# Performance work log

Hardware: AMD Instinct MI355X
Metric: run time of the kernel (lower is better)

The kernel has to match this reference:

```python
import jax, jax.numpy as jnp
import numpy as np

D_MODEL = 1024
N_HEADS = 16
D_K = D_MODEL // N_HEADS


def setup_inputs() -> dict:
    key = jax.random.key(0)
    ks = jax.random.split(key, 12)
    B, S = 4, 2048
    sc = 1.0 / np.sqrt(D_MODEL)
    inp = {
        "query": jax.random.normal(ks[0], (B, S, D_MODEL), jnp.float32),
        "key": jax.random.normal(ks[1], (B, S, D_MODEL), jnp.float32),
        "value": jax.random.normal(ks[2], (B, S, D_MODEL), jnp.float32),
        "Wq": jax.random.normal(ks[3], (D_MODEL, D_MODEL), jnp.float32) * sc,
        "bq": jnp.zeros((D_MODEL,), jnp.float32),
        "Wk": jax.random.normal(ks[4], (D_MODEL, D_MODEL), jnp.float32) * sc,
        "bk": jnp.zeros((D_MODEL,), jnp.float32),
        "Wv": jax.random.normal(ks[5], (D_MODEL, D_MODEL), jnp.float32) * sc,
        "bv": jnp.zeros((D_MODEL,), jnp.float32),
        "Wo": jax.random.normal(ks[6], (D_MODEL, D_MODEL), jnp.float32) * sc,
        "bo": jnp.zeros((D_MODEL,), jnp.float32),
    }
    return inp


def _split_heads(x):
    B, S, _ = x.shape
    return x.reshape(B, S, N_HEADS, D_K).transpose(0, 2, 1, 3)  # [B,H,S,Dk]


def reference(query, key, value, Wq, bq, Wk, bk, Wv, bv, Wo, bo):
    q = _split_heads(query @ Wq.T + bq)
    k = _split_heads(key @ Wk.T + bk)
    v = _split_heads(value @ Wv.T + bv)
    scores = jnp.einsum("bhqd,bhkd->bhqk", q, k) / jnp.sqrt(jnp.float32(D_K))
    # Faithful to source: softmax over dim=1 (the HEAD axis), a quirk of the original.
    probs = jax.nn.softmax(scores, axis=1)
    attn = jnp.einsum("bhqk,bhkd->bhqd", probs, v)
    B, H, S, Dk = attn.shape
    combined = attn.transpose(0, 2, 1, 3).reshape(B, S, H * Dk)
    return combined @ Wo.T + bo
```

## Files before the change

kernel.cpp:

```cpp
#include <hip/hip_runtime.h>
#include <stdint.h>

typedef __attribute__((ext_vector_type(8))) short bf16x8;
typedef __attribute__((ext_vector_type(4))) float f32x4;
typedef __attribute__((ext_vector_type(4))) float fl4;
typedef __attribute__((ext_vector_type(4))) unsigned short u16x4;
typedef __attribute__((ext_vector_type(8))) unsigned short u16x8;

constexpr int SEQ = 2048;
constexpr int DMODEL = 1024;
constexpr int NH = 16;
constexpr int DKH = 64;
constexpr float SEXP = 0.18033688f;

__device__ __forceinline__ unsigned short f2bf(float x) {
  union { float f; uint32_t u; } c;
  c.f = x;
  uint32_t u = c.u;
  u += 0x7FFFu + ((u >> 16) & 1u);
  return (unsigned short)(u >> 16);
}

__device__ __forceinline__ float bf2f(unsigned short u) {
  union { uint32_t u; float f; } c;
  c.u = ((uint32_t)u) << 16;
  return c.f;
}

__device__ __forceinline__ uint32_t cvtpk(float lo, float hi) {
  uint32_t r;
  asm("v_cvt_pk_bf16_f32 %0, %1, %2" : "=v"(r) : "v"(lo), "v"(hi));
  return r;
}

#if __has_builtin(__builtin_amdgcn_exp2f)
__device__ __forceinline__ float fexp2(float x) { return __builtin_amdgcn_exp2f(x); }
#else
__device__ __forceinline__ float fexp2(float x) { return exp2f(x); }
#endif

__device__ __forceinline__ int swz(int row) { return (row & 3) ^ ((row >> 2) & 3); }

__device__ __forceinline__ void gload16(const unsigned short* g, unsigned short* l) {
  __builtin_amdgcn_global_load_lds((const __attribute__((address_space(1))) void*)g,
                                   (__attribute__((address_space(3))) void*)l, 16, 0, 0);
}

__global__ __launch_bounds__(256) void cvtk(
    const float* __restrict__ s0, const float* __restrict__ s1, const float* __restrict__ s2,
    unsigned short* __restrict__ d0, unsigned short* __restrict__ d1, unsigned short* __restrict__ d2) {
  const float* s = blockIdx.y == 0 ? s0 : blockIdx.y == 1 ? s1 : s2;
  unsigned short* d = blockIdx.y == 0 ? d0 : blockIdx.y == 1 ? d1 : d2;
  const size_t i = ((size_t)blockIdx.x * 256 + threadIdx.x) * 8;
  fl4 a = *(const fl4*)(s + i);
  fl4 c = *(const fl4*)(s + i + 4);
  u16x8 r;
#pragma unroll
  for (int j = 0; j < 4; ++j) { r[j] = f2bf(a[j]); r[4 + j] = f2bf(c[j]); }
  *(u16x8*)(d + i) = r;
}

__global__ __launch_bounds__(256) void cvt1(
    const float* __restrict__ s, unsigned short* __restrict__ d) {
  const size_t i = ((size_t)blockIdx.x * 256 + threadIdx.x) * 8;
  fl4 a = *(const fl4*)(s + i);
  fl4 c = *(const fl4*)(s + i + 4);
  u16x8 r;
#pragma unroll
  for (int j = 0; j < 4; ++j) { r[j] = f2bf(a[j]); r[4 + j] = f2bf(c[j]); }
  *(u16x8*)(d + i) = r;
}

template <int EPI>
__global__ __launch_bounds__(256, 2) void gemm3(
    const unsigned short* __restrict__ A, const unsigned short* __restrict__ Bb,
    const float* __restrict__ bias, void* __restrict__ Cp, float ascale) {
  constexpr int K = DMODEL;
  constexpr int N = DMODEL;
  __shared__ unsigned short As[2][128 * 32];
  __shared__ unsigned short Bs[2][128 * 32];
  const int tid = threadIdx.x;
  const int wave = tid >> 6, lane = tid & 63;
  const int g = lane >> 4, ln = lane & 15;
  const int o = blockIdx.x;
  const int x = o & 7, idx = o >> 3;
  const int r0 = (x * 8 + (idx & 7)) * 128;
  const int c0 = (idx >> 3) * 128;
  const int wr = (wave >> 1) * 64, wc = (wave & 1) * 64;

  f32x4 acc[4][4] = {};

  auto STAGE = [&](int buf, int kt) {
#pragma unroll
    for (int i = 0; i < 2; ++i) {
      const int row = i * 64 + (tid >> 2);
      const int cs = ((tid & 3) ^ swz(row)) * 8;
      gload16(A + (size_t)(r0 + row) * K + kt + cs, As[buf] + (i * 256 + wave * 64) * 8);
      gload16(Bb + (size_t)(c0 + row) * K + kt + cs, Bs[buf] + (i * 256 + wave * 64) * 8);
    }
  };

  STAGE(0, 0);
  __syncthreads();

  for (int t = 0; t < K / 32; ++t) {
    const int buf = t & 1;
    if (t + 1 < K / 32) STAGE(buf ^ 1, (t + 1) * 32);
    bf16x8 af[4], bfr[4];
#pragma unroll
    for (int m = 0; m < 4; ++m) {
      const int row = wr + m * 16 + ln;
      af[m] = *(const bf16x8*)(As[buf] + row * 32 + ((g ^ swz(row)) * 8));
    }
#pragma unroll
    for (int n = 0; n < 4; ++n) {
      const int row = wc + n * 16 + ln;
      bfr[n] = *(const bf16x8*)(Bs[buf] + row * 32 + ((g ^ swz(row)) * 8));
    }
#pragma unroll
    for (int m = 0; m < 4; ++m)
#pragma unroll
      for (int n = 0; n < 4; ++n)
        acc[m][n] = __builtin_amdgcn_mfma_f32_16x16x32_bf16(af[m], bfr[n], acc[m][n], 0, 0, 0);
    __syncthreads();
  }

#pragma unroll
  for (int m = 0; m < 4; ++m) {
    const int row = r0 + wr + m * 16 + g * 4;
#pragma unroll
    for (int n = 0; n < 4; ++n) {
      const int col = c0 + wc + n * 16 + ln;
      const float bv = bias[col];
      f32x4 v = acc[m][n];
      if (EPI == 2) {
        float* C = (float*)Cp;
#pragma unroll
        for (int r = 0; r < 4; ++r) C[(size_t)(row + r) * N + col] = (v[r] + bv) * ascale;
      } else if (EPI == 0) {
        unsigned short* C = (unsigned short*)Cp;
#pragma unroll
        for (int r = 0; r < 4; ++r) C[(size_t)(row + r) * N + col] = f2bf((v[r] + bv) * ascale);
      } else {
        unsigned short* Vt = (unsigned short*)Cp;
        const int bb = row >> 11, sl = row & 2047;
        const int h = col >> 6, d = col & 63;
        const int sp = (sl & ~31) | (((sl >> 2) & 3) << 3) | (((sl >> 4) & 1) << 2);
        u16x4 pk;
#pragma unroll
        for (int r = 0; r < 4; ++r) pk[r] = f2bf((v[r] + bv) * ascale);
        *(u16x4*)(Vt + ((size_t)((bb * NH + h) * DKH + d)) * SEQ + sp) = pk;
      }
    }
  }
}

__global__ __launch_bounds__(256, 3) void denomk(
    const unsigned short* __restrict__ Qp, const unsigned short* __restrict__ Kp,
    unsigned short* __restrict__ rDb) {
  __shared__ unsigned short Ks[2][128 * 64];
  const int tid = threadIdx.x, wave = tid >> 6, lane = tid & 63;
  const int g = lane >> 4, ln = lane & 15;
  const int o = blockIdx.x;
  const int l = (o & 7) * 256 + (o >> 3);
  const int b = l >> 9;
  const int qg = (l >> 4) & 31;
  const int kvg = l & 15;
  const int q0 = qg * 64, kvb = kvg * 128;
  const int kw = wave * 32;

  auto STAGE = [&](int buf, int h) {
#pragma unroll
    for (int i = 0; i < 4; ++i) {
      const int s = i * 256 + tid;
      const int row = s >> 3, c = s & 7;
      gload16(Kp + (size_t)(b * SEQ + kvb + row) * DMODEL + h * DKH + ((c ^ (row & 7)) * 8),
              Ks[buf] + (i * 256 + wave * 64) * 8);
    }
  };

  f32x4 psum[2][4] = {};

  STAGE(0, 0);
  __syncthreads();

  for (int h = 0; h < NH; ++h) {
    const int buf = h & 1;
    if (h + 1 < NH) STAGE(buf ^ 1, h + 1);
    bf16x8 qf[2][4];
#pragma unroll
    for (int ks = 0; ks < 2; ++ks)
#pragma unroll
      for (int n = 0; n < 4; ++n)
        qf[ks][n] = *(const bf16x8*)(Qp + (size_t)(b * SEQ + q0 + n * 16 + ln) * DMODEL + h * DKH + ks * 32 + g * 8);
    bf16x8 kf[2][2];
#pragma unroll
    for (int m = 0; m < 2; ++m)
#pragma unroll
      for (int ks = 0; ks < 2; ++ks) {
        const int r = kw + m * 16 + ln;
        const int cc = ks * 4 + g;
        kf[m][ks] = *(const bf16x8*)(Ks[buf] + r * 64 + ((cc ^ (r & 7)) * 8));
      }
    f32x4 s[2][4] = {};
#pragma unroll
    for (int m = 0; m < 2; ++m)
#pragma unroll
      for (int n = 0; n < 4; ++n) {
        s[m][n] = __builtin_amdgcn_mfma_f32_16x16x32_bf16(kf[m][0], qf[0][n], s[m][n], 0, 0, 0);
        s[m][n] = __builtin_amdgcn_mfma_f32_16x16x32_bf16(kf[m][1], qf[1][n], s[m][n], 0, 0, 0);
      }
#pragma unroll
    for (int m = 0; m < 2; ++m)
#pragma unroll
      for (int n = 0; n < 4; ++n)
#pragma unroll
        for (int r = 0; r < 4; ++r) psum[m][n][r] += fexp2(s[m][n][r]);
    __syncthreads();
  }

#pragma unroll
  for (int m = 0; m < 2; ++m)
#pragma unroll
    for (int n = 0; n < 4; ++n) {
      u16x4 st;
#pragma unroll
      for (int r = 0; r < 4; ++r) st[r] = f2bf(1.0f / psum[m][n][r]);
      *(u16x4*)(rDb + (size_t)(b * SEQ + q0 + n * 16 + ln) * SEQ + kvb + kw + m * 16 + g * 4) = st;
    }
}

__global__ __launch_bounds__(256, 4) void flashk(
    const unsigned short* __restrict__ Qp, const unsigned short* __restrict__ Kp,
    const unsigned short* __restrict__ Vt, const unsigned short* __restrict__ rDb,
    unsigned short* __restrict__ Ab) {
  __shared__ unsigned short Ks[2][64 * 64];
  __shared__ unsigned short Vs[2][64 * 64];
  const int tid = threadIdx.x, wave = tid >> 6, lane = tid & 63;
  const int g = lane >> 4, ln = lane & 15;
  const int o = blockIdx.x;
  const int l = (o & 7) * 128 + (o >> 3);
  const int b = l >> 8;
  const int h = (l >> 4) & 15;
  const int q0 = (l & 15) * 128 + wave * 32;

  bf16x8 qf[2][2];
#pragma unroll
  for (int ks = 0; ks < 2; ++ks)
#pragma unroll
    for (int n = 0; n < 2; ++n)
      qf[ks][n] = *(const bf16x8*)(Qp + (size_t)(b * SEQ + q0 + n * 16 + ln) * DMODEL + h * DKH + ks * 32 + g * 8);

  f32x4 ao[4][2] = {};
  const size_t rbase0 = (size_t)(b * SEQ + q0 + ln) * SEQ;
  const size_t kbase = (size_t)(b * SEQ) * DMODEL + h * DKH;
  const size_t vbase = (size_t)((b * NH + h) * DKH) * SEQ;

  auto STAGE = [&](int buf, int kv0) {
#pragma unroll
    for (int i = 0; i < 2; ++i) {
      const int s = i * 256 + tid;
      const int row = s >> 3, c = s & 7;
      gload16(Kp + kbase + (size_t)(kv0 + row) * DMODEL + ((c ^ (row & 7)) * 8),
              Ks[buf] + (i * 256 + wave * 64) * 8);
    }
#pragma unroll
    for (int i = 0; i < 2; ++i) {
      const int s = i * 256 + tid;
      const int row = s >> 3, c = s & 7;
      gload16(Vt + vbase + (size_t)row * SEQ + kv0 + ((c ^ (row & 7)) * 8),
              Vs[buf] + (i * 256 + wave * 64) * 8);
    }
  };

  STAGE(0, 0);
  __syncthreads();

  for (int t = 0; t < SEQ / 64; ++t) {
    const int kv0 = t * 64, buf = t & 1;
    if (t + 1 < SEQ / 64) STAGE(buf ^ 1, kv0 + 64);

#pragma unroll
    for (int si = 0; si < 2; ++si) {
      u16x4 rdq[2][2];
#pragma unroll
      for (int n = 0; n < 2; ++n)
#pragma unroll
        for (int m = 0; m < 2; ++m)
          rdq[n][m] = *(const u16x4*)(rDb + rbase0 + (size_t)(n * 16) * SEQ + kv0 + si * 32 + m * 16 + g * 4);

      f32x4 s2[2][2] = {};
      __builtin_amdgcn_s_setprio(1);
#pragma unroll
      for (int m = 0; m < 2; ++m) {
        const int row = si * 32 + m * 16 + ln;
#pragma unroll
        for (int ks = 0; ks < 2; ++ks) {
          const int cc = ks * 4 + g;
          bf16x8 kf = *(const bf16x8*)(Ks[buf] + row * 64 + ((cc ^ (row & 7)) * 8));
#pragma unroll
          for (int n = 0; n < 2; ++n)
            s2[m][n] = __builtin_amdgcn_mfma_f32_16x16x32_bf16(kf, qf[ks][n], s2[m][n], 0, 0, 0);
        }
      }
      __builtin_amdgcn_s_setprio(0);

      bf16x8 pfr[2];
#pragma unroll
      for (int n = 0; n < 2; ++n) {
        uint32_t dw[4];
#pragma unroll
        for (int m = 0; m < 2; ++m) {
          float p0 = fexp2(s2[m][n][0]) * bf2f(rdq[n][m][0]);
          float p1 = fexp2(s2[m][n][1]) * bf2f(rdq[n][m][1]);
          float p2 = fexp2(s2[m][n][2]) * bf2f(rdq[n][m][2]);
          float p3 = fexp2(s2[m][n][3]) * bf2f(rdq[n][m][3]);
          dw[m * 2 + 0] = cvtpk(p0, p1);
          dw[m * 2 + 1] = cvtpk(p2, p3);
        }
        union { uint32_t u[4]; bf16x8 v; } cv;
        cv.u[0] = dw[0]; cv.u[1] = dw[1]; cv.u[2] = dw[2]; cv.u[3] = dw[3];
        pfr[n] = cv.v;
      }

      __builtin_amdgcn_s_setprio(1);
#pragma unroll
      for (int dt = 0; dt < 4; ++dt) {
        const int vrow = dt * 16 + ln;
        const int vc = si * 4 + g;
        bf16x8 vf = *(const bf16x8*)(Vs[buf] + vrow * 64 + ((vc ^ (vrow & 7)) * 8));
#pragma unroll
        for (int n = 0; n < 2; ++n)
          ao[dt][n] = __builtin_amdgcn_mfma_f32_16x16x32_bf16(vf, pfr[n], ao[dt][n], 0, 0, 0);
      }
      __builtin_amdgcn_s_setprio(0);
    }
    __syncthreads();
  }

#pragma unroll
  for (int dt = 0; dt < 4; ++dt)
#pragma unroll
    for (int n = 0; n < 2; ++n) {
      u16x4 st;
#pragma unroll
      for (int r = 0; r < 4; ++r) st[r] = f2bf(ao[dt][n][r]);
      *(u16x4*)(Ab + (size_t)(b * SEQ + q0 + n * 16 + ln) * DMODEL + h * DKH + dt * 16 + g * 4) = st;
    }
}

extern "C" void kernel_launch(void* const* d_in, const int* in_sizes, int n_in,
                              void* d_out, int out_size, void* d_ws, size_t ws_size,
                              hipStream_t stream) {
  (void)in_sizes; (void)n_in; (void)out_size; (void)ws_size;
  const float* query = (const float*)d_in[0];
  const float* key   = (const float*)d_in[1];
  const float* value = (const float*)d_in[2];
  const float* Wq = (const float*)d_in[3];
  const float* bq = (const float*)d_in[4];
  const float* Wk = (const float*)d_in[5];
  const float* bk = (const float*)d_in[6];
  const float* Wv = (const float*)d_in[7];
  const float* bv = (const float*)d_in[8];
  const float* Wo = (const float*)d_in[9];
  const float* bo = (const float*)d_in[10];

  uint8_t* ws = (uint8_t*)d_ws;
  const size_t SZ = (size_t)4 * SEQ * DMODEL * 2;
  const size_t WSZ = (size_t)DMODEL * DMODEL;
  unsigned short* Xv = (unsigned short*)(ws);
  unsigned short* Qp = (unsigned short*)(ws);
  unsigned short* Wob = (unsigned short*)(ws);
  unsigned short* Kp = (unsigned short*)(ws + SZ);
  unsigned short* Vt = (unsigned short*)(ws + 2 * SZ);
  unsigned short* Ab = (unsigned short*)(ws + 3 * SZ);
  unsigned short* Wqb = Ab;
  unsigned short* Wkb = Ab + WSZ;
  unsigned short* Wvb = Ab + 2 * WSZ;
  unsigned short* Xq = (unsigned short*)d_out;
  unsigned short* Xk = (unsigned short*)d_out + (size_t)4 * SEQ * DMODEL;
  unsigned short* rDb = (unsigned short*)d_out;

  cvtk<<<dim3(4096, 3), 256, 0, stream>>>(query, key, value, Xq, Xk, Xv);
  cvtk<<<dim3(512, 3), 256, 0, stream>>>(Wq, Wk, Wv, Wqb, Wkb, Wvb);
  gemm3<1><<<512, 256, 0, stream>>>(Xv, Wvb, bv, Vt, 1.0f);
  gemm3<0><<<512, 256, 0, stream>>>(Xq, Wqb, bq, Qp, SEXP);
  gemm3<0><<<512, 256, 0, stream>>>(Xk, Wkb, bk, Kp, 1.0f);
  denomk<<<2048, 256, 0, stream>>>(Qp, Kp, rDb);
  flashk<<<1024, 256, 0, stream>>>(Qp, Kp, Vt, rDb, Ab);
  cvt1<<<512, 256, 0, stream>>>(Wo, Wob);
  gemm3<2><<<512, 256, 0, stream>>>(Ab, Wob, bo, (float*)d_out, 1.0f);
}
```

Measured before the change: 418.5 us.

## Fuse fp32-to-bf16 input conversion into a single batched QKV projection GEMM

Removes the separate activation conversion kernel. The new GEMM loads fp32 query/key/value rows directly, converts them to bf16 in registers and writes them into shared memory, with the global loads for the next tile issued before the MFMAs. The three Q/K/V projection launches are merged into one 1536-block grid that selects input, weights, bias and epilogue per segment. This avoids writing and re-reading bf16 copies of the activations and cuts launch count, at the cost of twice the global read bytes for A, more registers for staging, and a conversion step on the GEMM's critical path.

```diff
diff --git a/kernel.cpp b/kernel.cpp
--- a/kernel.cpp
+++ b/kernel.cpp
@@ -71,10 +71,120 @@
   *(u16x8*)(d + i) = r;
 }
 
-template <int EPI>
-__global__ __launch_bounds__(256, 2) void gemm3(
+__global__ __launch_bounds__(256, 2) void gemmqkv(
+    const float* __restrict__ Xq, const float* __restrict__ Xk, const float* __restrict__ Xv,
+    const unsigned short* __restrict__ Wb,
+    const float* __restrict__ bq, const float* __restrict__ bk, const float* __restrict__ bv,
+    unsigned short* __restrict__ Qp, unsigned short* __restrict__ Kp, unsigned short* __restrict__ Vt) {
+  constexpr int K = DMODEL;
+  __shared__ unsigned short As[2][128 * 32];
+  __shared__ unsigned short Bs[2][128 * 32];
+  const int tid = threadIdx.x;
+  const int wave = tid >> 6, lane = tid & 63;
+  const int g = lane >> 4, ln = lane & 15;
+  const int o = blockIdx.x;
+  const int x = o & 7, j = o >> 3;
+  const int si = j >> 5, w = j & 31;
+  const int seg = si >> 1;
+  const int r0 = (x * 8 + (si & 1) * 4 + (w & 3)) * 128;
+  const int c0 = (w >> 2) * 128;
+  const int wr = (wave >> 1) * 64, wc = (wave & 1) * 64;
+  const int arow = tid >> 2, cc = tid & 3;
+
+  const float* A = seg == 0 ? Xq : seg == 1 ? Xk : Xv;
+  const unsigned short* Bw = Wb + (size_t)seg * DMODEL * DMODEL;
+  const float* bias = seg == 0 ? bq : seg == 1 ? bk : bv;
+  const float ascale = seg == 0 ? SEXP : 1.0f;
+
+  f32x4 acc[4][4] = {};
+  fl4 ar[2][2];
+
+  auto LOADA = [&](int kt) {
+#pragma unroll
+    for (int i = 0; i < 2; ++i) {
+      const size_t ao = (size_t)(r0 + arow + i * 64) * K + kt + cc * 8;
+      ar[i][0] = *(const fl4*)(A + ao);
+      ar[i][1] = *(const fl4*)(A + ao + 4);
+    }
+  };
+  auto WRITEA = [&](int buf) {
+#pragma unroll
+    for (int i = 0; i < 2; ++i) {
+      const int row = arow + i * 64;
+      const int ch = (cc ^ swz(row)) * 8;
+      union { uint32_t u[4]; u16x8 v; } pk;
+      pk.u[0] = cvtpk(ar[i][0][0], ar[i][0][1]);
+      pk.u[1] = cvtpk(ar[i][0][2], ar[i][0][3]);
+      pk.u[2] = cvtpk(ar[i][1][0], ar[i][1][1]);
+      pk.u[3] = cvtpk(ar[i][1][2], ar[i][1][3]);
+      *(u16x8*)(As[buf] + row * 32 + ch) = pk.v;
+    }
+  };
+  auto STAGEB = [&](int buf, int kt) {
+#pragma unroll
+    for (int i = 0; i < 2; ++i) {
+      const int row = i * 64 + (tid >> 2);
+      const int cs = ((tid & 3) ^ swz(row)) * 8;
+      gload16(Bw + (size_t)(c0 + row) * K + kt + cs, Bs[buf] + (i * 256 + wave * 64) * 8);
+    }
+  };
+
+  LOADA(0);
+  WRITEA(0);
+  STAGEB(0, 0);
+  __syncthreads();
+
+  for (int t = 0; t < K / 32; ++t) {
+    const int buf = t & 1;
+    if (t + 1 < K / 32) { LOADA((t + 1) * 32); STAGEB(buf ^ 1, (t + 1) * 32); }
+    bf16x8 af[4], bfr[4];
+#pragma unroll
+    for (int m = 0; m < 4; ++m) {
+      const int row = wr + m * 16 + ln;
+      af[m] = *(const bf16x8*)(As[buf] + row * 32 + ((g ^ swz(row)) * 8));
+    }
+#pragma unroll
+    for (int n = 0; n < 4; ++n) {
+      const int row = wc + n * 16 + ln;
+      bfr[n] = *(const bf16x8*)(Bs[buf] + row * 32 + ((g ^ swz(row)) * 8));
+    }
+#pragma unroll
+    for (int m = 0; m < 4; ++m)
+#pragma unroll
+      for (int n = 0; n < 4; ++n)
+        acc[m][n] = __builtin_amdgcn_mfma_f32_16x16x32_bf16(af[m], bfr[n], acc[m][n], 0, 0, 0);
+    if (t + 1 < K / 32) WRITEA(buf ^ 1);
+    __syncthreads();
+  }
+
+#pragma unroll
+  for (int m = 0; m < 4; ++m) {
+    const int row = r0 + wr + m * 16 + g * 4;
+#pragma unroll
+    for (int n = 0; n < 4; ++n) {
+      const int col = c0 + wc + n * 16 + ln;
+      const float bvv = bias[col];
+      f32x4 v = acc[m][n];
+      if (seg < 2) {
+        unsigned short* C = seg == 0 ? Qp : Kp;
+#pragma unroll
+        for (int r = 0; r < 4; ++r) C[(size_t)(row + r) * DMODEL + col] = f2bf((v[r] + bvv) * ascale);
+      } else {
+        const int bb = row >> 11, sl = row & 2047;
+        const int h = col >> 6, d = col & 63;
+        const int sp = (sl & ~31) | (((sl >> 2) & 3) << 3) | (((sl >> 4) & 1) << 2);
+        u16x4 pk;
+#pragma unroll
+        for (int r = 0; r < 4; ++r) pk[r] = f2bf(v[r] + bvv);
+        *(u16x4*)(Vt + ((size_t)((bb * NH + h) * DKH + d)) * SEQ + sp) = pk;
+      }
+    }
+  }
+}
+
+__global__ __launch_bounds__(256, 2) void gemmout(
     const unsigned short* __restrict__ A, const unsigned short* __restrict__ Bb,
-    const float* __restrict__ bias, void* __restrict__ Cp, float ascale) {
+    const float* __restrict__ bias, float* __restrict__ Cp) {
   constexpr int K = DMODEL;
   constexpr int N = DMODEL;
   __shared__ unsigned short As[2][128 * 32];
@@ -131,26 +241,10 @@
 #pragma unroll
     for (int n = 0; n < 4; ++n) {
       const int col = c0 + wc + n * 16 + ln;
-      const float bv = bias[col];
+      const float bvv = bias[col];
       f32x4 v = acc[m][n];
-      if (EPI == 2) {
-        float* C = (float*)Cp;
-#pragma unroll
-        for (int r = 0; r < 4; ++r) C[(size_t)(row + r) * N + col] = (v[r] + bv) * ascale;
-      } else if (EPI == 0) {
-        unsigned short* C = (unsigned short*)Cp;
-#pragma unroll
-        for (int r = 0; r < 4; ++r) C[(size_t)(row + r) * N + col] = f2bf((v[r] + bv) * ascale);
-      } else {
-        unsigned short* Vt = (unsigned short*)Cp;
-        const int bb = row >> 11, sl = row & 2047;
-        const int h = col >> 6, d = col & 63;
-        const int sp = (sl & ~31) | (((sl >> 2) & 3) << 3) | (((sl >> 4) & 1) << 2);
-        u16x4 pk;
-#pragma unroll
-        for (int r = 0; r < 4; ++r) pk[r] = f2bf((v[r] + bv) * ascale);
-        *(u16x4*)(Vt + ((size_t)((bb * NH + h) * DKH + d)) * SEQ + sp) = pk;
-      }
+#pragma unroll
+      for (int r = 0; r < 4; ++r) Cp[(size_t)(row + r) * N + col] = v[r] + bvv;
     }
   }
 }
@@ -368,26 +462,20 @@
   uint8_t* ws = (uint8_t*)d_ws;
   const size_t SZ = (size_t)4 * SEQ * DMODEL * 2;
   const size_t WSZ = (size_t)DMODEL * DMODEL;
-  unsigned short* Xv = (unsigned short*)(ws);
-  unsigned short* Qp = (unsigned short*)(ws);
+  unsigned short* Qp  = (unsigned short*)(ws);
   unsigned short* Wob = (unsigned short*)(ws);
-  unsigned short* Kp = (unsigned short*)(ws + SZ);
-  unsigned short* Vt = (unsigned short*)(ws + 2 * SZ);
-  unsigned short* Ab = (unsigned short*)(ws + 3 * SZ);
-  unsigned short* Wqb = Ab;
-  unsigned short* Wkb = Ab + WSZ;
-  unsigned short* Wvb = Ab + 2 * WSZ;
-  unsigned short* Xq = (unsigned short*)d_out;
-  unsigned short* Xk = (unsigned short*)d_out + (size_t)4 * SEQ * DMODEL;
+  unsigned short* Kp  = (unsigned short*)(ws + SZ);
+  unsigned short* Vt  = (unsigned short*)(ws + 2 * SZ);
+  unsigned short* Wqb = (unsigned short*)(ws + 3 * SZ);
+  unsigned short* Wkb = Wqb + WSZ;
+  unsigned short* Wvb = Wqb + 2 * WSZ;
+  unsigned short* Ab  = (unsigned short*)(ws + 3 * SZ);
   unsigned short* rDb = (unsigned short*)d_out;
 
-  cvtk<<<dim3(4096, 3), 256, 0, stream>>>(query, key, value, Xq, Xk, Xv);
   cvtk<<<dim3(512, 3), 256, 0, stream>>>(Wq, Wk, Wv, Wqb, Wkb, Wvb);
-  gemm3<1><<<512, 256, 0, stream>>>(Xv, Wvb, bv, Vt, 1.0f);
-  gemm3<0><<<512, 256, 0, stream>>>(Xq, Wqb, bq, Qp, SEXP);
-  gemm3<0><<<512, 256, 0, stream>>>(Xk, Wkb, bk, Kp, 1.0f);
+  gemmqkv<<<1536, 256, 0, stream>>>(query, key, value, Wqb, bq, bk, bv, Qp, Kp, Vt);
   denomk<<<2048, 256, 0, stream>>>(Qp, Kp, rDb);
   flashk<<<1024, 256, 0, stream>>>(Qp, Kp, Vt, rDb, Ab);
   cvt1<<<512, 256, 0, stream>>>(Wo, Wob);
-  gemm3<2><<<512, 256, 0, stream>>>(Ab, Wob, bo, (float*)d_out, 1.0f);
-}
+  gemmout<<<512, 256, 0, stream>>>(Ab, Wob, bo, (float*)d_out);
+}
```

After: 388.6 us (median of 3 runs). 7.1% less time.
